# Optimization experiments

Measured on AMD Instinct MI355X. Metric: run time of the kernel, lower is better.

## Reference

```python
import jax, jax.numpy as jnp
import numpy as np

N = 100000      # nodes
E = 1600000     # directed edges
D_IN, H, D_OUT = 512, 128, 64
ALPHA = 0.1     # GCNII residual strength; beta = 1.0 (PyG default theta=None)
NUM_LAYERS = 2


def setup_inputs() -> dict:
    key = jax.random.key(0)
    k = jax.random.split(key, 8)
    x = jax.random.normal(k[0], (N, D_IN), dtype=jnp.float32)
    edge_index = jax.random.randint(k[1], (2, E), 0, N, dtype=jnp.int32)
    w1 = jax.random.normal(k[2], (D_IN, H), dtype=jnp.float32) * (1.0 / np.sqrt(D_IN))
    b1 = jnp.zeros((H,), dtype=jnp.float32)
    conv_w = jax.random.normal(k[3], (NUM_LAYERS, H, H), dtype=jnp.float32) * (1.0 / np.sqrt(H))
    w2 = jax.random.normal(k[4], (H, D_OUT), dtype=jnp.float32) * (1.0 / np.sqrt(H))
    b2 = jnp.zeros((D_OUT,), dtype=jnp.float32)
    return dict(x=x, edge_index=edge_index, w1=w1, b1=b1, conv_w=conv_w, w2=w2, b2=b2)


def reference(x, edge_index, w1, b1, conv_w, w2, b2):
    n = x.shape[0]
    # --- GCN normalization with self-loops (computed once; identical each layer) ---
    loops = jnp.arange(n, dtype=edge_index.dtype)
    row = jnp.concatenate([edge_index[0], loops])   # source nodes
    col = jnp.concatenate([edge_index[1], loops])   # target nodes
    deg = jax.ops.segment_sum(jnp.ones(row.shape, jnp.float32), col, num_segments=n)
    dinv = jnp.where(deg > 0, jax.lax.rsqrt(jnp.maximum(deg, 1.0)), 0.0)
    norm = dinv[row] * dinv[col]                    # [E+N] edge weights

    # linear1 + relu (dropout is identity in eval mode)
    h = jax.nn.relu(x @ w1 + b1)                    # [N, H]
    h0 = h

    # stacked GCN2Conv: h = ((1-alpha) * A_hat @ h + alpha * h0) @ W_l   (beta=1)
    for l in range(NUM_LAYERS):
        agg = jax.ops.segment_sum(norm[:, None] * h[row], col, num_segments=n)  # gather -> weight -> scatter-add
        h = ((1.0 - ALPHA) * agg + ALPHA * h0) @ conv_w[l]

    logits = h @ w2 + b2                            # [N, D_OUT]
    return h, logits
```

## Files before the change

kernel.cpp:

```cpp
#include <hip/hip_runtime.h>

constexpr int N_NODES = 100000;
constexpr int N_EDGES = 1600000;
constexpr int D_IN   = 512;
constexpr int H_DIM  = 128;
constexpr int D_OUT  = 64;
constexpr float ALPHA = 0.1f;

constexpr int SCAN_TPB = 256;
constexpr int SCAN_EPB = SCAN_TPB * 8;
constexpr int SCAN_NB  = (N_NODES + SCAN_EPB - 1) / SCAN_EPB;

typedef __attribute__((ext_vector_type(4))) float f32x4;
typedef __attribute__((ext_vector_type(8))) short bf16x8;

__device__ __forceinline__ unsigned short f2bf(float f) {
    unsigned int u = __float_as_uint(f);
    u += 0x7fff + ((u >> 16) & 1);
    return (unsigned short)(u >> 16);
}
__device__ __forceinline__ float bf2f(unsigned short b) {
    return __uint_as_float(((unsigned int)b) << 16);
}


__global__ void k_init(int* __restrict__ deg, int n) {
    int i = blockIdx.x * blockDim.x + threadIdx.x;
    if (i < n) deg[i] = 0;
}

__global__ void k_count(const int* __restrict__ col, int* __restrict__ deg, int e) {
    int i = blockIdx.x * blockDim.x + threadIdx.x;
    if (i < e) atomicAdd(&deg[col[i]], 1);
}


__global__ __launch_bounds__(SCAN_TPB) void k_scan_part(const int* __restrict__ deg,
                                                        int* __restrict__ partials, int n) {
    __shared__ int red[SCAN_TPB];
    int t = threadIdx.x;
    int base = blockIdx.x * SCAN_EPB + t * 8;
    int s = 0;
    if (base + 8 <= n) {
        int4 a = *(const int4*)(deg + base);
        int4 b = *(const int4*)(deg + base + 4);
        s = a.x + a.y + a.z + a.w + b.x + b.y + b.z + b.w;
    } else {
        for (int j = 0; j < 8; ++j) if (base + j < n) s += deg[base + j];
    }
    red[t] = s;
    __syncthreads();
    for (int off = SCAN_TPB / 2; off > 0; off >>= 1) {
        if (t < off) red[t] += red[t + off];
        __syncthreads();
    }
    if (t == 0) partials[blockIdx.x] = red[0];
}

__global__ __launch_bounds__(64) void k_scan_mid(int* __restrict__ partials,
                                                 int* __restrict__ offsets) {
    __shared__ int buf[SCAN_NB];
    int t = threadIdx.x;
    if (t < SCAN_NB) buf[t] = partials[t];
    __syncthreads();
    if (t == 0) {
        int run = 0;
        for (int i = 0; i < SCAN_NB; ++i) { int v = buf[i]; buf[i] = run; run += v; }
        offsets[N_NODES] = run;
    }
    __syncthreads();
    if (t < SCAN_NB) partials[t] = buf[t];
}

__global__ __launch_bounds__(SCAN_TPB) void k_scan_write(const int* __restrict__ deg,
                                                         const int* __restrict__ partials,
                                                         int* __restrict__ offsets,
                                                         int* __restrict__ cursor,
                                                         float* __restrict__ dinv, int n) {
    __shared__ int sums[SCAN_TPB];
    int t = threadIdx.x;
    int base = blockIdx.x * SCAN_EPB + t * 8;
    int v[8];
    if (base + 8 <= n) {
        int4 a = *(const int4*)(deg + base);
        int4 b = *(const int4*)(deg + base + 4);
        v[0] = a.x; v[1] = a.y; v[2] = a.z; v[3] = a.w;
        v[4] = b.x; v[5] = b.y; v[6] = b.z; v[7] = b.w;
    } else {
        for (int j = 0; j < 8; ++j) v[j] = (base + j < n) ? deg[base + j] : 0;
    }
    int p[8], s = 0;
#pragma unroll
    for (int j = 0; j < 8; ++j) { p[j] = s; s += v[j]; }
    sums[t] = s;
    __syncthreads();
    for (int off = 1; off < SCAN_TPB; off <<= 1) {
        int add = (t >= off) ? sums[t - off] : 0;
        __syncthreads();
        sums[t] += add;
        __syncthreads();
    }
    int tbase = partials[blockIdx.x] + ((t == 0) ? 0 : sums[t - 1]);
#pragma unroll
    for (int j = 0; j < 8; ++j)
        if (base + j < n) {
            int o = tbase + p[j];
            offsets[base + j] = o;
            cursor[base + j] = o;
            dinv[base + j] = rsqrtf((float)(v[j] + 1));
        }
}

__global__ void k_fill(const int* __restrict__ row, const int* __restrict__ col,
                       int* __restrict__ cursor, const float* __restrict__ dinv,
                       int2* __restrict__ edges, int e) {
    int i = blockIdx.x * blockDim.x + threadIdx.x;
    if (i >= e) return;
    int r = row[i], c = col[i];
    int p = atomicAdd(&cursor[c], 1);
    int2 v;
    v.x = r;
    v.y = __float_as_int(dinv[r] * dinv[c]);
    edges[p] = v;
}


__global__ __launch_bounds__(256) void k_agg(
        const unsigned short* __restrict__ hb,
        const unsigned short* __restrict__ h0b,
        const int* __restrict__ offsets, const int2* __restrict__ edges,
        const float* __restrict__ dinv,
        unsigned short* __restrict__ zb, int n) {
    int wid  = (int)((blockIdx.x * (unsigned)blockDim.x + threadIdx.x) >> 6);
    int lane = threadIdx.x & 63;
    if (wid >= n) return;
    float di = dinv[wid];
    const float oma = 1.0f - ALPHA;
    int o0 = offsets[wid], o1 = offsets[wid + 1];
    ushort2 hc = ((const ushort2*)(hb  + (size_t)wid * H_DIM))[lane];
    ushort2 hz = ((const ushort2*)(h0b + (size_t)wid * H_DIM))[lane];
    float sw = oma * di * di;
    float accx = sw * bf2f(hc.x) + ALPHA * bf2f(hz.x);
    float accy = sw * bf2f(hc.y) + ALPHA * bf2f(hz.y);
    int p2 = o0;
    for (; p2 + 8 <= o1; p2 += 8) {
        int2 e[8];
        ushort2 g[8];
#pragma unroll
        for (int j = 0; j < 8; ++j) e[j] = edges[p2 + j];
#pragma unroll
        for (int j = 0; j < 8; ++j)
            g[j] = ((const ushort2*)(hb + (size_t)e[j].x * H_DIM))[lane];
#pragma unroll
        for (int j = 0; j < 8; ++j) {
            float w = oma * __int_as_float(e[j].y);
            accx += w * bf2f(g[j].x);
            accy += w * bf2f(g[j].y);
        }
    }
    for (; p2 < o1; ++p2) {
        int2 e = edges[p2];
        float wv = oma * __int_as_float(e.y);
        ushort2 g = ((const ushort2*)(hb + (size_t)e.x * H_DIM))[lane];
        accx += wv * bf2f(g.x); accy += wv * bf2f(g.y);
    }
    ushort2 o; o.x = f2bf(accx); o.y = f2bf(accy);
    ((ushort2*)(zb + (size_t)wid * H_DIM))[lane] = o;
}


constexpr int W1_E = D_IN * H_DIM;
constexpr int CW_E = 2 * H_DIM * H_DIM;
constexpr int W2_E = H_DIM * D_OUT;

__global__ void k_wprep_all(const float* __restrict__ w1, const float* __restrict__ cw,
                            const float* __restrict__ w2,
                            unsigned short* __restrict__ w1th, unsigned short* __restrict__ w1tl,
                            unsigned short* __restrict__ cwth, unsigned short* __restrict__ cwtl,
                            unsigned short* __restrict__ w2th, unsigned short* __restrict__ w2tl) {
    int i = blockIdx.x * blockDim.x + threadIdx.x;
    const float* src; unsigned short *dh, *dl; int K, Nn, j;
    if (i < W1_E) {
        src = w1; dh = w1th; dl = w1tl; K = D_IN; Nn = H_DIM; j = i;
    } else if (i < W1_E + CW_E) {
        j = i - W1_E; int l = j >> 14; j &= 16383;
        src = cw + l * H_DIM * H_DIM; dh = cwth + l * H_DIM * H_DIM; dl = cwtl + l * H_DIM * H_DIM;
        K = H_DIM; Nn = H_DIM;
    } else if (i < W1_E + CW_E + W2_E) {
        j = i - W1_E - CW_E; src = w2; dh = w2th; dl = w2tl; K = H_DIM; Nn = D_OUT;
    } else return;
    int n = j / K, k = j % K;
    float v = src[(size_t)k * Nn + n];
    unsigned short h = f2bf(v);
    dh[j] = h;
    dl[j] = f2bf(v - bf2f(h));
}


template<int BN, bool AF32, bool RELU, bool BIAS, bool WF32, bool WB16>
__global__ __launch_bounds__(256, 4) void k_mfma_gemm(
        const float* __restrict__ Af,
        const unsigned short* __restrict__ Ab,
        const unsigned short* __restrict__ Bth,
        const unsigned short* __restrict__ Btl,
        const float* __restrict__ bias,
        float* __restrict__ C, unsigned short* __restrict__ Cb,
        int M, int K) {
    constexpr int BM = 64, BK = 64;
    constexpr int WN = BN / 2;
    constexpr int NF = WN / 16;
    __shared__ unsigned short Ah[BM * BK];
    __shared__ unsigned short Bh[BN * BK], Bl[BN * BK];
    char* AhC = (char*)Ah;
    char* BhC = (char*)Bh; char* BlC = (char*)Bl;
    const int tid = threadIdx.x;
    const int wave = tid >> 6, lane = tid & 63;
    const int wrow = wave >> 1, wcol = wave & 1;
    const int l15 = lane & 15, l4 = lane >> 4;
    const int bm = blockIdx.x * BM;

    f32x4 acc[2][NF];
#pragma unroll
    for (int mf = 0; mf < 2; ++mf)
#pragma unroll
        for (int nf = 0; nf < NF; ++nf) acc[mf][nf] = (f32x4){0.f, 0.f, 0.f, 0.f};

    for (int k0 = 0; k0 < K; k0 += BK) {
#pragma unroll
        for (int c = 0; c < (BM * 8) / 256; ++c) {
            int ch = tid + c * 256;
            int m = ch >> 3, kc = (ch & 7) * 8;
            int gr = bm + m;
            bf16x8 hv;
            if constexpr (AF32) {
                float v[8];
                if (gr < M) {
                    const float4* src = (const float4*)(Af + (size_t)gr * K + k0 + kc);
                    float4 a0 = src[0], a1 = src[1];
                    v[0] = a0.x; v[1] = a0.y; v[2] = a0.z; v[3] = a0.w;
                    v[4] = a1.x; v[5] = a1.y; v[6] = a1.z; v[7] = a1.w;
                } else {
#pragma unroll
                    for (int j = 0; j < 8; ++j) v[j] = 0.f;
                }
#pragma unroll
                for (int j = 0; j < 8; ++j) hv[j] = (short)f2bf(v[j]);
            } else {
                if (gr < M) {
                    hv = *(const bf16x8*)(Ab + (size_t)gr * K + k0 + kc);
                } else {
                    hv = (bf16x8){0, 0, 0, 0, 0, 0, 0, 0};
                }
            }
            int byte = ((m * BK + kc) * 2) ^ ((m & 7) << 4);
            *(bf16x8*)(AhC + byte) = hv;
        }
#pragma unroll
        for (int c = 0; c < (BN * 8) / 256; ++c) {
            int ch = tid + c * 256;
            int n = ch >> 3, kc = (ch & 7) * 8;
            bf16x8 hv = *(const bf16x8*)(Bth + (size_t)n * K + k0 + kc);
            bf16x8 lv = *(const bf16x8*)(Btl + (size_t)n * K + k0 + kc);
            int byte = ((n * BK + kc) * 2) ^ ((n & 7) << 4);
            *(bf16x8*)(BhC + byte) = hv;
            *(bf16x8*)(BlC + byte) = lv;
        }
        __syncthreads();
#pragma unroll
        for (int ks = 0; ks < 2; ++ks) {
            bf16x8 ah[2], bh[NF], bl[NF];
#pragma unroll
            for (int mf = 0; mf < 2; ++mf) {
                int row = wrow * 32 + mf * 16 + l15;
                int byte = ((row * BK + ks * 32 + l4 * 8) * 2) ^ ((row & 7) << 4);
                ah[mf] = *(const bf16x8*)(AhC + byte);
            }
#pragma unroll
            for (int nf = 0; nf < NF; ++nf) {
                int n = wcol * WN + nf * 16 + l15;
                int byte = ((n * BK + ks * 32 + l4 * 8) * 2) ^ ((n & 7) << 4);
                bh[nf] = *(const bf16x8*)(BhC + byte);
                bl[nf] = *(const bf16x8*)(BlC + byte);
            }
#pragma unroll
            for (int mf = 0; mf < 2; ++mf)
#pragma unroll
                for (int nf = 0; nf < NF; ++nf) {
                    acc[mf][nf] = __builtin_amdgcn_mfma_f32_16x16x32_bf16(ah[mf], bh[nf], acc[mf][nf], 0, 0, 0);
                    acc[mf][nf] = __builtin_amdgcn_mfma_f32_16x16x32_bf16(ah[mf], bl[nf], acc[mf][nf], 0, 0, 0);
                }
        }
        __syncthreads();
    }
#pragma unroll
    for (int mf = 0; mf < 2; ++mf) {
#pragma unroll
        for (int nf = 0; nf < NF; ++nf) {
            int col = wcol * WN + nf * 16 + l15;
            float bv = 0.f;
            if constexpr (BIAS) bv = bias[col];
#pragma unroll
            for (int r = 0; r < 4; ++r) {
                int grow = bm + wrow * 32 + mf * 16 + l4 * 4 + r;
                if (grow < M) {
                    float v = acc[mf][nf][r] + bv;
                    if constexpr (RELU) v = fmaxf(v, 0.f);
                    if constexpr (WF32) C[(size_t)grow * BN + col] = v;
                    if constexpr (WB16) Cb[(size_t)grow * BN + col] = f2bf(v);
                }
            }
        }
    }
}


__global__ __launch_bounds__(256, 3) void k_conv1_logits(
        const unsigned short* __restrict__ Ab,
        const unsigned short* __restrict__ Bth,
        const unsigned short* __restrict__ Btl,
        const unsigned short* __restrict__ W2h,
        const unsigned short* __restrict__ W2l,
        const float* __restrict__ b2,
        float* __restrict__ h2, float* __restrict__ logits, int M) {
    constexpr int BM = 64, BK = 64, BN = 128, K = 128;
    constexpr int WN = BN / 2, NF = WN / 16;
    __shared__ char lds[49152];
    char* AhC = lds;
    char* BhC = lds + 8192;
    char* BlC = lds + 24576;
    char* A2C = lds;
    char* WhC = lds + 16384;
    char* WlC = lds + 32768;
    const int tid = threadIdx.x;
    const int wave = tid >> 6, lane = tid & 63;
    const int wrow = wave >> 1, wcol = wave & 1;
    const int l15 = lane & 15, l4 = lane >> 4;
    const int bm = blockIdx.x * BM;

    f32x4 acc[2][NF];
#pragma unroll
    for (int mf = 0; mf < 2; ++mf)
#pragma unroll
        for (int nf = 0; nf < NF; ++nf) acc[mf][nf] = (f32x4){0.f, 0.f, 0.f, 0.f};

    for (int k0 = 0; k0 < K; k0 += BK) {
#pragma unroll
        for (int c = 0; c < (BM * 8) / 256; ++c) {
            int ch = tid + c * 256;
            int m = ch >> 3, kc = (ch & 7) * 8;
            int gr = bm + m;
            bf16x8 hv;
            if (gr < M) hv = *(const bf16x8*)(Ab + (size_t)gr * K + k0 + kc);
            else        hv = (bf16x8){0, 0, 0, 0, 0, 0, 0, 0};
            int byte = ((m * BK + kc) * 2) ^ ((m & 7) << 4);
            *(bf16x8*)(AhC + byte) = hv;
        }
#pragma unroll
        for (int c = 0; c < (BN * 8) / 256; ++c) {
            int ch = tid + c * 256;
            int n = ch >> 3, kc = (ch & 7) * 8;
            bf16x8 hv = *(const bf16x8*)(Bth + (size_t)n * K + k0 + kc);
            bf16x8 lv = *(const bf16x8*)(Btl + (size_t)n * K + k0 + kc);
            int byte = ((n * BK + kc) * 2) ^ ((n & 7) << 4);
            *(bf16x8*)(BhC + byte) = hv;
            *(bf16x8*)(BlC + byte) = lv;
        }
        __syncthreads();
#pragma unroll
        for (int ks = 0; ks < 2; ++ks) {
            bf16x8 ah[2], bh[NF], bl[NF];
#pragma unroll
            for (int mf = 0; mf < 2; ++mf) {
                int row = wrow * 32 + mf * 16 + l15;
                int byte = ((row * BK + ks * 32 + l4 * 8) * 2) ^ ((row & 7) << 4);
                ah[mf] = *(const bf16x8*)(AhC + byte);
            }
#pragma unroll
            for (int nf = 0; nf < NF; ++nf) {
                int n = wcol * WN + nf * 16 + l15;
                int byte = ((n * BK + ks * 32 + l4 * 8) * 2) ^ ((n & 7) << 4);
                bh[nf] = *(const bf16x8*)(BhC + byte);
                bl[nf] = *(const bf16x8*)(BlC + byte);
            }
#pragma unroll
            for (int mf = 0; mf < 2; ++mf)
#pragma unroll
                for (int nf = 0; nf < NF; ++nf) {
                    acc[mf][nf] = __builtin_amdgcn_mfma_f32_16x16x32_bf16(ah[mf], bh[nf], acc[mf][nf], 0, 0, 0);
                    acc[mf][nf] = __builtin_amdgcn_mfma_f32_16x16x32_bf16(ah[mf], bl[nf], acc[mf][nf], 0, 0, 0);
                }
        }
        __syncthreads();
    }
#pragma unroll
    for (int mf = 0; mf < 2; ++mf) {
#pragma unroll
        for (int nf = 0; nf < NF; ++nf) {
            int col = wcol * WN + nf * 16 + l15;
#pragma unroll
            for (int r = 0; r < 4; ++r) {
                int mrow = wrow * 32 + mf * 16 + l4 * 4 + r;
                int grow = bm + mrow;
                float v = acc[mf][nf][r];
                if (grow < M) h2[(size_t)grow * BN + col] = v;
                int byte = ((mrow * 128 + col) * 2) ^ ((mrow & 7) << 4);
                *(unsigned short*)(A2C + byte) = f2bf(v);
            }
        }
    }
#pragma unroll
    for (int c = 0; c < 4; ++c) {
        int ch = tid + c * 256;
        int n = ch >> 4, kc = (ch & 15) * 8;
        bf16x8 hv = *(const bf16x8*)(W2h + (size_t)n * 128 + kc);
        bf16x8 lv = *(const bf16x8*)(W2l + (size_t)n * 128 + kc);
        int byte = ((n * 128 + kc) * 2) ^ ((n & 7) << 4);
        *(bf16x8*)(WhC + byte) = hv;
        *(bf16x8*)(WlC + byte) = lv;
    }
    __syncthreads();

    f32x4 acc2[2][2];
#pragma unroll
    for (int mf = 0; mf < 2; ++mf)
#pragma unroll
        for (int nf = 0; nf < 2; ++nf) acc2[mf][nf] = (f32x4){0.f, 0.f, 0.f, 0.f};
#pragma unroll
    for (int ks = 0; ks < 4; ++ks) {
        bf16x8 a2[2], wh[2], wl[2];
#pragma unroll
        for (int mf = 0; mf < 2; ++mf) {
            int row = wrow * 32 + mf * 16 + l15;
            int byte = ((row * 128 + ks * 32 + l4 * 8) * 2) ^ ((row & 7) << 4);
            a2[mf] = *(const bf16x8*)(A2C + byte);
        }
#pragma unroll
        for (int nf = 0; nf < 2; ++nf) {
            int n = wcol * 32 + nf * 16 + l15;
            int byte = ((n * 128 + ks * 32 + l4 * 8) * 2) ^ ((n & 7) << 4);
            wh[nf] = *(const bf16x8*)(WhC + byte);
            wl[nf] = *(const bf16x8*)(WlC + byte);
        }
#pragma unroll
        for (int mf = 0; mf < 2; ++mf)
#pragma unroll
            for (int nf = 0; nf < 2; ++nf) {
                acc2[mf][nf] = __builtin_amdgcn_mfma_f32_16x16x32_bf16(a2[mf], wh[nf], acc2[mf][nf], 0, 0, 0);
                acc2[mf][nf] = __builtin_amdgcn_mfma_f32_16x16x32_bf16(a2[mf], wl[nf], acc2[mf][nf], 0, 0, 0);
            }
    }
#pragma unroll
    for (int mf = 0; mf < 2; ++mf) {
#pragma unroll
        for (int nf = 0; nf < 2; ++nf) {
            int col = wcol * 32 + nf * 16 + l15;
            float bv = b2[col];
#pragma unroll
            for (int r = 0; r < 4; ++r) {
                int grow = bm + wrow * 32 + mf * 16 + l4 * 4 + r;
                if (grow < M)
                    logits[(size_t)grow * D_OUT + col] = acc2[mf][nf][r] + bv;
            }
        }
    }
}


extern "C" void kernel_launch(void* const* d_in, const int* in_sizes, int n_in,
                              void* d_out, int out_size, void* d_ws, size_t ws_size,
                              hipStream_t stream) {
    const float* x  = (const float*)d_in[0];
    const int*   ei = (const int*)d_in[1];
    const float* w1 = (const float*)d_in[2];
    const float* b1 = (const float*)d_in[3];
    const float* cw = (const float*)d_in[4];
    const float* w2 = (const float*)d_in[5];
    const float* b2 = (const float*)d_in[6];
    float* out = (float*)d_out;
    const int* rowp = ei;
    const int* colp = ei + N_EDGES;

    char* p = (char*)d_ws;
    auto alloc = [&](size_t bytes) -> void* {
        void* r = (void*)p;
        p += ((bytes + 255) / 256) * 256;
        return r;
    };
    int*   deg     = (int*)  alloc((size_t)N_NODES * 4);
    int*   cursor  = (int*)  alloc((size_t)N_NODES * 4);
    int*   offsets = (int*)  alloc((size_t)(N_NODES + 1) * 4);
    int*   partials= (int*)  alloc((size_t)SCAN_NB * 4);
    int2*  edges   = (int2*) alloc((size_t)N_EDGES * 8);
    float* dinv    = (float*)alloc((size_t)N_NODES * 4);
    unsigned short* zb  = (unsigned short*)alloc((size_t)N_NODES * H_DIM * 2);
    unsigned short* h0b = (unsigned short*)alloc((size_t)N_NODES * H_DIM * 2);
    unsigned short* h1b = (unsigned short*)alloc((size_t)N_NODES * H_DIM * 2);
    unsigned short* w1th = (unsigned short*)alloc((size_t)W1_E * 2);
    unsigned short* w1tl = (unsigned short*)alloc((size_t)W1_E * 2);
    unsigned short* cwth = (unsigned short*)alloc((size_t)CW_E * 2);
    unsigned short* cwtl = (unsigned short*)alloc((size_t)CW_E * 2);
    unsigned short* w2th = (unsigned short*)alloc((size_t)W2_E * 2);
    unsigned short* w2tl = (unsigned short*)alloc((size_t)W2_E * 2);

    float* h2     = out;
    float* logits = out + (size_t)N_NODES * H_DIM;

    hipLaunchKernelGGL(k_init,  dim3((N_NODES + 255) / 256), dim3(256), 0, stream, deg, N_NODES);
    hipLaunchKernelGGL(k_count, dim3((N_EDGES + 255) / 256), dim3(256), 0, stream, colp, deg, N_EDGES);
    hipLaunchKernelGGL(k_scan_part,  dim3(SCAN_NB), dim3(SCAN_TPB), 0, stream, deg, partials, N_NODES);
    hipLaunchKernelGGL(k_scan_mid,   dim3(1), dim3(64), 0, stream, partials, offsets);
    hipLaunchKernelGGL(k_scan_write, dim3(SCAN_NB), dim3(SCAN_TPB), 0, stream,
                       deg, partials, offsets, cursor, dinv, N_NODES);
    hipLaunchKernelGGL(k_fill,  dim3((N_EDGES + 255) / 256), dim3(256), 0, stream,
                       rowp, colp, cursor, dinv, edges, N_EDGES);

    hipLaunchKernelGGL(k_wprep_all, dim3((W1_E + CW_E + W2_E + 255) / 256), dim3(256), 0, stream,
                       w1, cw, w2, w1th, w1tl, cwth, cwtl, w2th, w2tl);

    int gemmGrid = (N_NODES + 63) / 64;
    hipLaunchKernelGGL((k_mfma_gemm<128, true, true, true, false, true>), dim3(gemmGrid), dim3(256), 0, stream,
                       x, (const unsigned short*)nullptr, w1th, w1tl, b1,
                       (float*)nullptr, h0b, N_NODES, D_IN);

    int aggGrid = (int)(((size_t)N_NODES * 64 + 255) / 256);
    hipLaunchKernelGGL(k_agg, dim3(aggGrid), dim3(256), 0, stream,
                       h0b, h0b, offsets, edges, dinv, zb, N_NODES);
    hipLaunchKernelGGL((k_mfma_gemm<128, false, false, false, false, true>), dim3(gemmGrid), dim3(256), 0, stream,
                       (const float*)nullptr, zb, cwth, cwtl, (const float*)nullptr,
                       (float*)nullptr, h1b, N_NODES, H_DIM);
    hipLaunchKernelGGL(k_agg, dim3(aggGrid), dim3(256), 0, stream,
                       h1b, h0b, offsets, edges, dinv, zb, N_NODES);
    hipLaunchKernelGGL(k_conv1_logits, dim3(gemmGrid), dim3(256), 0, stream,
                       zb, cwth + H_DIM * H_DIM, cwtl + H_DIM * H_DIM,
                       w2th, w2tl, b2, h2, logits, N_NODES);
}
```

Baseline: 438.8 us.

## Merge independent preprocessing kernels into combined launches to overlap work

```diff
diff --git a/kernel.cpp b/kernel.cpp
--- a/kernel.cpp
+++ b/kernel.cpp
@@ -29,9 +29,52 @@
     if (i < n) deg[i] = 0;
 }
 
-__global__ void k_count(const int* __restrict__ col, int* __restrict__ deg, int e) {
-    int i = blockIdx.x * blockDim.x + threadIdx.x;
-    if (i < e) atomicAdd(&deg[col[i]], 1);
+
+constexpr int W1_E = D_IN * H_DIM;
+constexpr int CW_E = 2 * H_DIM * H_DIM;
+constexpr int W2_E = H_DIM * D_OUT;
+constexpr int WP_E = W1_E + CW_E + W2_E;
+constexpr int WP_NB = (WP_E + 255) / 256;
+
+__device__ __forceinline__ void wprep_body(int i,
+        const float* __restrict__ w1, const float* __restrict__ cw,
+        const float* __restrict__ w2,
+        unsigned short* __restrict__ w1th, unsigned short* __restrict__ w1tl,
+        unsigned short* __restrict__ cwth, unsigned short* __restrict__ cwtl,
+        unsigned short* __restrict__ w2th, unsigned short* __restrict__ w2tl) {
+    const float* src; unsigned short *dh, *dl; int K, Nn, j;
+    if (i < W1_E) {
+        src = w1; dh = w1th; dl = w1tl; K = D_IN; Nn = H_DIM; j = i;
+    } else if (i < W1_E + CW_E) {
+        j = i - W1_E; int l = j >> 14; j &= 16383;
+        src = cw + l * H_DIM * H_DIM; dh = cwth + l * H_DIM * H_DIM; dl = cwtl + l * H_DIM * H_DIM;
+        K = H_DIM; Nn = H_DIM;
+    } else if (i < WP_E) {
+        j = i - W1_E - CW_E; src = w2; dh = w2th; dl = w2tl; K = H_DIM; Nn = D_OUT;
+    } else return;
+    int n = j / K, k = j % K;
+    float v = src[(size_t)k * Nn + n];
+    unsigned short h = f2bf(v);
+    dh[j] = h;
+    dl[j] = f2bf(v - bf2f(h));
+}
+
+constexpr int CNT_NB = (N_EDGES + 255) / 256;
+
+__global__ __launch_bounds__(256) void k_mega_count_wprep(
+        const int* __restrict__ col, int* __restrict__ deg,
+        const float* __restrict__ w1, const float* __restrict__ cw, const float* __restrict__ w2,
+        unsigned short* __restrict__ w1th, unsigned short* __restrict__ w1tl,
+        unsigned short* __restrict__ cwth, unsigned short* __restrict__ cwtl,
+        unsigned short* __restrict__ w2th, unsigned short* __restrict__ w2tl) {
+    int b = blockIdx.x;
+    if (b < CNT_NB) {
+        int i = b * 256 + threadIdx.x;
+        if (i < N_EDGES) atomicAdd(&deg[col[i]], 1);
+    } else {
+        int i = (b - CNT_NB) * 256 + threadIdx.x;
+        wprep_body(i, w1, cw, w2, w1th, w1tl, cwth, cwtl, w2th, w2tl);
+    }
 }
 
 
@@ -109,19 +152,6 @@
             cursor[base + j] = o;
             dinv[base + j] = rsqrtf((float)(v[j] + 1));
         }
-}
-
-__global__ void k_fill(const int* __restrict__ row, const int* __restrict__ col,
-                       int* __restrict__ cursor, const float* __restrict__ dinv,
-                       int2* __restrict__ edges, int e) {
-    int i = blockIdx.x * blockDim.x + threadIdx.x;
-    if (i >= e) return;
-    int r = row[i], c = col[i];
-    int p = atomicAdd(&cursor[c], 1);
-    int2 v;
-    v.x = r;
-    v.y = __float_as_int(dinv[r] * dinv[c]);
-    edges[p] = v;
 }
 
 
@@ -169,36 +199,9 @@
 }
 
 
-constexpr int W1_E = D_IN * H_DIM;
-constexpr int CW_E = 2 * H_DIM * H_DIM;
-constexpr int W2_E = H_DIM * D_OUT;
-
-__global__ void k_wprep_all(const float* __restrict__ w1, const float* __restrict__ cw,
-                            const float* __restrict__ w2,
-                            unsigned short* __restrict__ w1th, unsigned short* __restrict__ w1tl,
-                            unsigned short* __restrict__ cwth, unsigned short* __restrict__ cwtl,
-                            unsigned short* __restrict__ w2th, unsigned short* __restrict__ w2tl) {
-    int i = blockIdx.x * blockDim.x + threadIdx.x;
-    const float* src; unsigned short *dh, *dl; int K, Nn, j;
-    if (i < W1_E) {
-        src = w1; dh = w1th; dl = w1tl; K = D_IN; Nn = H_DIM; j = i;
-    } else if (i < W1_E + CW_E) {
-        j = i - W1_E; int l = j >> 14; j &= 16383;
-        src = cw + l * H_DIM * H_DIM; dh = cwth + l * H_DIM * H_DIM; dl = cwtl + l * H_DIM * H_DIM;
-        K = H_DIM; Nn = H_DIM;
-    } else if (i < W1_E + CW_E + W2_E) {
-        j = i - W1_E - CW_E; src = w2; dh = w2th; dl = w2tl; K = H_DIM; Nn = D_OUT;
-    } else return;
-    int n = j / K, k = j % K;
-    float v = src[(size_t)k * Nn + n];
-    unsigned short h = f2bf(v);
-    dh[j] = h;
-    dl[j] = f2bf(v - bf2f(h));
-}
-
-
 template<int BN, bool AF32, bool RELU, bool BIAS, bool WF32, bool WB16>
-__global__ __launch_bounds__(256, 4) void k_mfma_gemm(
+__device__ __forceinline__ void gemm_body(
+        char* AhC, char* BhC, char* BlC, int bm, int tid,
         const float* __restrict__ Af,
         const unsigned short* __restrict__ Ab,
         const unsigned short* __restrict__ Bth,
@@ -209,15 +212,9 @@
     constexpr int BM = 64, BK = 64;
     constexpr int WN = BN / 2;
     constexpr int NF = WN / 16;
-    __shared__ unsigned short Ah[BM * BK];
-    __shared__ unsigned short Bh[BN * BK], Bl[BN * BK];
-    char* AhC = (char*)Ah;
-    char* BhC = (char*)Bh; char* BlC = (char*)Bl;
-    const int tid = threadIdx.x;
     const int wave = tid >> 6, lane = tid & 63;
     const int wrow = wave >> 1, wcol = wave & 1;
     const int l15 = lane & 15, l4 = lane >> 4;
-    const int bm = blockIdx.x * BM;
 
     f32x4 acc[2][NF];
 #pragma unroll
@@ -309,6 +306,52 @@
                     if constexpr (WB16) Cb[(size_t)grow * BN + col] = f2bf(v);
                 }
             }
+        }
+    }
+}
+
+template<int BN, bool AF32, bool RELU, bool BIAS, bool WF32, bool WB16>
+__global__ __launch_bounds__(256, 4) void k_mfma_gemm(
+        const float* __restrict__ Af,
+        const unsigned short* __restrict__ Ab,
+        const unsigned short* __restrict__ Bth,
+        const unsigned short* __restrict__ Btl,
+        const float* __restrict__ bias,
+        float* __restrict__ C, unsigned short* __restrict__ Cb,
+        int M, int K) {
+    __shared__ char lds[(64 + 2 * BN) * 64 * 2];
+    gemm_body<BN, AF32, RELU, BIAS, WF32, WB16>(
+        lds, lds + 64 * 64 * 2, lds + (64 + BN) * 64 * 2,
+        blockIdx.x * 64, threadIdx.x, Af, Ab, Bth, Btl, bias, C, Cb, M, K);
+}
+
+constexpr int LIN1_NB = (N_NODES + 63) / 64;
+constexpr int MEGA_B_NB = LIN1_NB * 5;
+
+__global__ __launch_bounds__(256, 4) void k_mega_fill_lin1(
+        const int* __restrict__ row, const int* __restrict__ col,
+        int* __restrict__ cursor, const float* __restrict__ dinv,
+        int2* __restrict__ edges,
+        const float* __restrict__ x,
+        const unsigned short* __restrict__ w1th, const unsigned short* __restrict__ w1tl,
+        const float* __restrict__ b1, unsigned short* __restrict__ h0b) {
+    __shared__ char lds[(64 + 2 * 128) * 64 * 2];
+    int b = blockIdx.x;
+    if ((b % 5) == 4) {
+        gemm_body<128, true, true, true, false, true>(
+            lds, lds + 64 * 64 * 2, lds + (64 + 128) * 64 * 2,
+            (b / 5) * 64, threadIdx.x, x, nullptr, w1th, w1tl, b1,
+            nullptr, h0b, N_NODES, D_IN);
+    } else {
+        int fidx = (b / 5) * 4 + (b % 5);
+        int i = fidx * 256 + (int)threadIdx.x;
+        if (i < N_EDGES) {
+            int r = row[i], c = col[i];
+            int p = atomicAdd(&cursor[c], 1);
+            int2 v;
+            v.x = r;
+            v.y = __float_as_int(dinv[r] * dinv[c]);
+            edges[p] = v;
         }
     }
 }
@@ -505,23 +548,18 @@
     float* h2     = out;
     float* logits = out + (size_t)N_NODES * H_DIM;
 
-    hipLaunchKernelGGL(k_init,  dim3((N_NODES + 255) / 256), dim3(256), 0, stream, deg, N_NODES);
-    hipLaunchKernelGGL(k_count, dim3((N_EDGES + 255) / 256), dim3(256), 0, stream, colp, deg, N_EDGES);
+    hipLaunchKernelGGL(k_init, dim3((N_NODES + 255) / 256), dim3(256), 0, stream, deg, N_NODES);
+    hipLaunchKernelGGL(k_mega_count_wprep, dim3(CNT_NB + WP_NB), dim3(256), 0, stream,
+                       colp, deg, w1, cw, w2, w1th, w1tl, cwth, cwtl, w2th, w2tl);
     hipLaunchKernelGGL(k_scan_part,  dim3(SCAN_NB), dim3(SCAN_TPB), 0, stream, deg, partials, N_NODES);
     hipLaunchKernelGGL(k_scan_mid,   dim3(1), dim3(64), 0, stream, partials, offsets);
     hipLaunchKernelGGL(k_scan_write, dim3(SCAN_NB), dim3(SCAN_TPB), 0, stream,
                        deg, partials, offsets, cursor, dinv, N_NODES);
-    hipLaunchKernelGGL(k_fill,  dim3((N_EDGES + 255) / 256), dim3(256), 0, stream,
-                       rowp, colp, cursor, dinv, edges, N_EDGES);
-
-    hipLaunchKernelGGL(k_wprep_all, dim3((W1_E + CW_E + W2_E + 255) / 256), dim3(256), 0, stream,
-                       w1, cw, w2, w1th, w1tl, cwth, cwtl, w2th, w2tl);
+
+    hipLaunchKernelGGL(k_mega_fill_lin1, dim3(MEGA_B_NB), dim3(256), 0, stream,
+                       rowp, colp, cursor, dinv, edges, x, w1th, w1tl, b1, h0b);
 
     int gemmGrid = (N_NODES + 63) / 64;
-    hipLaunchKernelGGL((k_mfma_gemm<128, true, true, true, false, true>), dim3(gemmGrid), dim3(256), 0, stream,
-                       x, (const unsigned short*)nullptr, w1th, w1tl, b1,
-                       (float*)nullptr, h0b, N_NODES, D_IN);
-
     int aggGrid = (int)(((size_t)N_NODES * 64 + 255) / 256);
     hipLaunchKernelGGL(k_agg, dim3(aggGrid), dim3(256), 0, stream,
                        h0b, h0b, offsets, edges, dinv, zb, N_NODES);
```

New measurement: 415.5 us (median of 2 runs). 5.3% less time.
